# Kernel optimization log

Hardware: AMD Instinct MI355X
Metric: run time of the kernel (lower is better)

Reference implementation:

```python
import jax, jax.numpy as jnp
import numpy as np
from jax import lax

B, S, L, E, H, V = 32, 64, 256, 64, 64, 6000


def setup_inputs() -> dict:
    key = jax.random.key(0)
    ks = jax.random.split(key, 8)
    inp = {
        "ids": jax.random.randint(ks[0], (B, S, L), 0, V, dtype=jnp.int32),
        "embed_table": jax.random.normal(ks[1], (V, E), jnp.float32) * 0.05,
        "Wk_f": jax.random.normal(ks[2], (E, 4 * H), jnp.float32) * 0.05,
        "Wr_f": jax.random.normal(ks[3], (H, 4 * H), jnp.float32) * 0.05,
        "b_f": jnp.zeros((4 * H,), jnp.float32),
        "Wk_b": jax.random.normal(ks[4], (E, 4 * H), jnp.float32) * 0.05,
        "Wr_b": jax.random.normal(ks[5], (H, 4 * H), jnp.float32) * 0.05,
        "b_b": jnp.zeros((4 * H,), jnp.float32),
    }
    return inp


def _lstm(xs, Wk, Wr, b):
    # xs: [L, N, E] -> hidden states [L, N, H]; Keras LSTM gate order i,f,c,o
    N = xs.shape[1]
    Hh = Wr.shape[0]
    pre = jnp.einsum('lne,eg->lng', xs, Wk) + b  # input projection once, outside scan

    def step(carry, zt):
        h, c = carry
        z = zt + h @ Wr
        i, f, g, o = jnp.split(z, 4, axis=-1)
        i = jax.nn.sigmoid(i)
        f = jax.nn.sigmoid(f)
        g = jnp.tanh(g)
        o = jax.nn.sigmoid(o)
        c = f * c + i * g
        h = o * jnp.tanh(c)
        return (h, c), h

    h0 = jnp.zeros((N, Hh), xs.dtype)
    _, hs = lax.scan(step, (h0, h0), pre)
    return hs


def reference(ids, embed_table, Wk_f, Wr_f, b_f, Wk_b, Wr_b, b_b):
    b, s, l = ids.shape
    e = embed_table.shape[1]
    h = Wr_f.shape[0]
    x = embed_table[ids]                      # [B,S,L,E]
    xs = x.reshape(b * s, l, e).transpose(1, 0, 2)  # [L, B*S, E]
    h_fwd = _lstm(xs, Wk_f, Wr_f, b_f)              # [L, N, H]
    h_bwd = _lstm(xs[::-1], Wk_b, Wr_b, b_b)[::-1]  # [L, N, H]
    out = jnp.concatenate([h_fwd, h_bwd], axis=-1)  # [L, N, 2H]
    return out.transpose(1, 0, 2).reshape(b, s, l, 2 * h)
```

## Files before the change

### kernel.cpp

```cpp
#include <hip/hip_runtime.h>

#define LL 256
#define EE 64
#define HH 64
#define GG 256
#define NSEQ 8
#define MROW 16
#define ROWP 72

typedef __bf16 bf16_t;
typedef bf16_t bf16x8 __attribute__((ext_vector_type(8)));
typedef float  f32x4  __attribute__((ext_vector_type(4)));

union BfPack {
    unsigned short u[8];
    bf16x8 v;
};

__device__ __forceinline__ unsigned short f2bf(float f) {
    return __builtin_bit_cast(unsigned short, (__bf16)f);
}

#define LOG2E 1.44269504088896340736f

__device__ __forceinline__ float sigm(float x) {
    float e = __builtin_amdgcn_exp2f(-LOG2E * x);
    return __builtin_amdgcn_rcpf(1.0f + e);
}
__device__ __forceinline__ float tanh_fast(float x) {
    float e = __builtin_amdgcn_exp2f((2.0f * LOG2E) * x);
    return 1.0f - 2.0f * __builtin_amdgcn_rcpf(e + 1.0f);
}

#define LGKM_BARRIER() asm volatile("s_waitcnt lgkmcnt(0)\n\ts_barrier" ::: "memory")

__global__ __launch_bounds__(256, 2)
void bilstm_mfma(const int* __restrict__ ids,
                 const float* __restrict__ embed,
                 const float* __restrict__ Wk_f, const float* __restrict__ Wr_f,
                 const float* __restrict__ b_f,
                 const float* __restrict__ Wk_b, const float* __restrict__ Wr_b,
                 const float* __restrict__ b_b,
                 float* __restrict__ out)
{
    const int dir = blockIdx.x >> 8;
    const int grp = blockIdx.x & 255;
    const int n0  = grp * NSEQ;
    const int tid  = threadIdx.x;
    const int w    = tid >> 6;
    const int lane = tid & 63;
    const int l15  = lane & 15;
    const int quad = lane >> 4;
    const int j    = w * 16 + l15;

    const float* Wk = dir ? Wk_b : Wk_f;
    const float* Wr = dir ? Wr_b : Wr_f;
    const float* bv = dir ? b_b  : b_f;

    __shared__ __align__(16) short s_x[2][MROW][ROWP];
    __shared__ __align__(16) short s_h[2][MROW][ROWP];
    __shared__ int s_ids[NSEQ][LL];

    for (int p = tid; p < NSEQ * LL; p += 256) {
        int m = p >> 8, t = p & 255;
        s_ids[m][t] = ids[(size_t)(n0 + m) * LL + t];
    }
    for (int p = tid; p < 2 * MROW * ROWP; p += 256) {
        (&s_h[0][0][0])[p] = 0;
        (&s_x[0][0][0])[p] = 0;
    }

    __syncthreads();

    bf16x8 bfrag[4][4];
    f32x4  biasC[4];
    #pragma unroll
    for (int tt = 0; tt < 4; ++tt) {
        int g = tt * 64 + j;
        float bb = bv[g];
        biasC[tt] = (f32x4){bb, bb, bb, bb};
        #pragma unroll
        for (int kc = 0; kc < 4; ++kc) {
            BfPack pk;
            #pragma unroll
            for (int e = 0; e < 8; ++e) {
                int kg = kc * 32 + quad * 8 + e;
                float v = (kg < 64) ? Wk[(size_t)kg * GG + g]
                                    : Wr[(size_t)(kg - 64) * GG + g];
                pk.u[e] = f2bf(v);
            }
            bfrag[tt][kc] = pk.v;
        }
    }

    {
        int t0 = dir ? (LL - 1) : 0;
        int m = tid >> 5, ep = tid & 31;
        int id = s_ids[m][t0];
        float2 xv = *(const float2*)&embed[(size_t)id * EE + 2 * ep];
        unsigned pk = (unsigned)f2bf(xv.x) | ((unsigned)f2bf(xv.y) << 16);
        *(unsigned*)&s_x[0][m][2 * ep] = pk;
    }
    __syncthreads();

    float c[4] = {0.f, 0.f, 0.f, 0.f};
    const f32x4 zero4 = (f32x4){0.f, 0.f, 0.f, 0.f};

    const int tstep = dir ? -(2 * HH) : (2 * HH);
    float* optr[4];
    {
        const int t0 = dir ? (LL - 1) : 0;
        #pragma unroll
        for (int r = 0; r < 4; ++r) {
            int m = quad * 4 + r;
            int mm = (m < NSEQ) ? m : 0;
            optr[r] = out + ((size_t)(n0 + mm) * LL + t0) * (2 * HH) + dir * HH + j;
        }
    }

    for (int ts = 0; ts < LL; ++ts) {
        const int rb = ts & 1, wb = (ts + 1) & 1;

        float2 px0;
        const int pm0 = tid >> 5, pe = tid & 31;
        const bool pf = (ts + 1 < LL);
        if (pf) {
            int tn = dir ? (LL - 2 - ts) : (ts + 1);
            px0 = *(const float2*)&embed[(size_t)s_ids[pm0][tn] * EE + 2 * pe];
        }

        bf16x8 ax0 = *(const bf16x8*)&s_x[rb][l15][quad * 8];
        bf16x8 ax1 = *(const bf16x8*)&s_x[rb][l15][32 + quad * 8];
        bf16x8 ah0 = *(const bf16x8*)&s_h[rb][l15][quad * 8];
        bf16x8 ah1 = *(const bf16x8*)&s_h[rb][l15][32 + quad * 8];

        f32x4 acc[4];
        #pragma unroll
        for (int tt = 0; tt < 4; ++tt) {
            f32x4 axc = __builtin_amdgcn_mfma_f32_16x16x32_bf16(ax0, bfrag[tt][0], biasC[tt], 0, 0, 0);
            axc = __builtin_amdgcn_mfma_f32_16x16x32_bf16(ax1, bfrag[tt][1], axc, 0, 0, 0);
            f32x4 ahc = __builtin_amdgcn_mfma_f32_16x16x32_bf16(ah0, bfrag[tt][2], zero4, 0, 0, 0);
            ahc = __builtin_amdgcn_mfma_f32_16x16x32_bf16(ah1, bfrag[tt][3], ahc, 0, 0, 0);
            acc[tt] = axc + ahc;
        }

        #pragma unroll
        for (int r = 0; r < 4; ++r) {
            float ig = sigm(acc[0][r]);
            float fg = sigm(acc[1][r]);
            float gg = tanh_fast(acc[2][r]);
            float og = sigm(acc[3][r]);
            c[r] = fg * c[r] + ig * gg;
            float hh = og * tanh_fast(c[r]);
            if (quad < 2) {
                *optr[r] = hh;
                s_h[wb][quad * 4 + r][j] = (short)f2bf(hh);
            }
            optr[r] += tstep;
        }

        if (pf) {
            unsigned pk0 = (unsigned)f2bf(px0.x) | ((unsigned)f2bf(px0.y) << 16);
            *(unsigned*)&s_x[wb][pm0][2 * pe] = pk0;
        }
        LGKM_BARRIER();
    }
}

extern "C" void kernel_launch(void* const* d_in, const int* in_sizes, int n_in,
                              void* d_out, int out_size, void* d_ws, size_t ws_size,
                              hipStream_t stream) {
    const int*   ids   = (const int*)d_in[0];
    const float* embed = (const float*)d_in[1];
    const float* Wk_f  = (const float*)d_in[2];
    const float* Wr_f  = (const float*)d_in[3];
    const float* b_f   = (const float*)d_in[4];
    const float* Wk_b  = (const float*)d_in[5];
    const float* Wr_b  = (const float*)d_in[6];
    const float* b_b   = (const float*)d_in[7];
    float* out = (float*)d_out;

    dim3 grid(512);
    dim3 block(256);
    bilstm_mfma<<<grid, block, 0, stream>>>(ids, embed,
                                            Wk_f, Wr_f, b_f,
                                            Wk_b, Wr_b, b_b,
                                            out);
}
```

Measured before the change: 476.3 us.

## Precompute vocab-level input projection table and pack 16 sequences per block

Adds a pre-kernel that computes embed_table @ Wk + b for every vocabulary entry and direction into a workspace table laid out to match the MFMA accumulator layout. The recurrent kernel then gathers precomputed gate pre-activations by token id and feeds them as the MFMA accumulator input, which halves the MFMAs per step. Each block now handles 16 sequences instead of 8, so all 16 MFMA rows are used, with 256 blocks at one block per CU. The trade-offs are a larger per-step gather (1 KB fp32 rows per token) and an extra kernel launch. The grid also halves, which reduces parallelism across CUs.

```diff
diff --git a/kernel.cpp b/kernel.cpp
--- a/kernel.cpp
+++ b/kernel.cpp
@@ -4,9 +4,10 @@
 #define EE 64
 #define HH 64
 #define GG 256
-#define NSEQ 8
-#define MROW 16
+#define VV 6000
+#define NSEQ 16
 #define ROWP 72
+#define VBLK 375
 
 typedef __bf16 bf16_t;
 typedef bf16_t bf16x8 __attribute__((ext_vector_type(8)));
@@ -34,17 +35,67 @@
 
 #define LGKM_BARRIER() asm volatile("s_waitcnt lgkmcnt(0)\n\ts_barrier" ::: "memory")
 
-__global__ __launch_bounds__(256, 2)
+__global__ __launch_bounds__(256)
+void embed_pre_kernel(const float* __restrict__ embed,
+                      const float* __restrict__ Wk_f, const float* __restrict__ b_f,
+                      const float* __restrict__ Wk_b, const float* __restrict__ b_b,
+                      float* __restrict__ pre)
+{
+    const int bid = blockIdx.x;
+    const int dir = bid / VBLK;
+    const int v0  = (bid % VBLK) * 16;
+    const float* Wk = dir ? Wk_b : Wk_f;
+    const float* bv = dir ? b_b  : b_f;
+    float* dst = pre + (size_t)dir * VV * GG;
+
+    const int tid = threadIdx.x;
+    const int r   = tid >> 4;
+    const int cg  = tid & 15;
+
+    __shared__ float sW[16][GG];
+    __shared__ float sE[16][17];
+
+    float acc[16];
+    #pragma unroll
+    for (int k = 0; k < 16; ++k) acc[k] = 0.f;
+
+    for (int ec = 0; ec < 4; ++ec) {
+        {
+            int er = tid >> 4;
+            int c0 = (tid & 15) * 16;
+            const float* src = &Wk[(size_t)(ec * 16 + er) * GG + c0];
+            *(float4*)&sW[er][c0 + 0]  = *(const float4*)(src + 0);
+            *(float4*)&sW[er][c0 + 4]  = *(const float4*)(src + 4);
+            *(float4*)&sW[er][c0 + 8]  = *(const float4*)(src + 8);
+            *(float4*)&sW[er][c0 + 12] = *(const float4*)(src + 12);
+            sE[er][tid & 15] = embed[(size_t)(v0 + er) * EE + ec * 16 + (tid & 15)];
+        }
+        __syncthreads();
+        #pragma unroll
+        for (int e = 0; e < 16; ++e) {
+            float xe = sE[r][e];
+            #pragma unroll
+            for (int k = 0; k < 16; ++k)
+                acc[k] += xe * sW[e][k * 16 + cg];
+        }
+        __syncthreads();
+    }
+    #pragma unroll
+    for (int k = 0; k < 16; ++k) {
+        int g = k * 16 + cg;
+        int pos = ((g >> 4) & 3) * 64 + (g & 15) * 4 + (g >> 6);
+        dst[(size_t)(v0 + r) * GG + pos] = acc[k] + bv[g];
+    }
+}
+
+__global__ __launch_bounds__(256, 1)
 void bilstm_mfma(const int* __restrict__ ids,
-                 const float* __restrict__ embed,
-                 const float* __restrict__ Wk_f, const float* __restrict__ Wr_f,
-                 const float* __restrict__ b_f,
-                 const float* __restrict__ Wk_b, const float* __restrict__ Wr_b,
-                 const float* __restrict__ b_b,
+                 const float* __restrict__ Wr_f, const float* __restrict__ Wr_b,
+                 const float* __restrict__ pre,
                  float* __restrict__ out)
 {
-    const int dir = blockIdx.x >> 8;
-    const int grp = blockIdx.x & 255;
+    const int dir = blockIdx.x >> 7;
+    const int grp = blockIdx.x & 127;
     const int n0  = grp * NSEQ;
     const int tid  = threadIdx.x;
     const int w    = tid >> 6;
@@ -53,95 +104,82 @@
     const int quad = lane >> 4;
     const int j    = w * 16 + l15;
 
-    const float* Wk = dir ? Wk_b : Wk_f;
     const float* Wr = dir ? Wr_b : Wr_f;
-    const float* bv = dir ? b_b  : b_f;
-
-    __shared__ __align__(16) short s_x[2][MROW][ROWP];
-    __shared__ __align__(16) short s_h[2][MROW][ROWP];
-    __shared__ int s_ids[NSEQ][LL];
+    const float* preT = pre + (size_t)dir * VV * GG;
+    const int coff = w * 64 + l15 * 4;
+
+    __shared__ __align__(16) short s_h[2][NSEQ][ROWP];
+    __shared__ int s_ids[NSEQ][LL + 1];
 
     for (int p = tid; p < NSEQ * LL; p += 256) {
         int m = p >> 8, t = p & 255;
         s_ids[m][t] = ids[(size_t)(n0 + m) * LL + t];
     }
-    for (int p = tid; p < 2 * MROW * ROWP; p += 256) {
+    for (int p = tid; p < 2 * NSEQ * ROWP; p += 256)
         (&s_h[0][0][0])[p] = 0;
-        (&s_x[0][0][0])[p] = 0;
-    }
 
     __syncthreads();
 
-    bf16x8 bfrag[4][4];
-    f32x4  biasC[4];
+    bf16x8 bfrag[4][2];
     #pragma unroll
     for (int tt = 0; tt < 4; ++tt) {
         int g = tt * 64 + j;
-        float bb = bv[g];
-        biasC[tt] = (f32x4){bb, bb, bb, bb};
-        #pragma unroll
-        for (int kc = 0; kc < 4; ++kc) {
+        #pragma unroll
+        for (int kc = 0; kc < 2; ++kc) {
             BfPack pk;
             #pragma unroll
             for (int e = 0; e < 8; ++e) {
                 int kg = kc * 32 + quad * 8 + e;
-                float v = (kg < 64) ? Wk[(size_t)kg * GG + g]
-                                    : Wr[(size_t)(kg - 64) * GG + g];
-                pk.u[e] = f2bf(v);
+                pk.u[e] = f2bf(Wr[(size_t)kg * GG + g]);
             }
             bfrag[tt][kc] = pk.v;
         }
     }
 
+    f32x4 curP[4];
     {
         int t0 = dir ? (LL - 1) : 0;
-        int m = tid >> 5, ep = tid & 31;
-        int id = s_ids[m][t0];
-        float2 xv = *(const float2*)&embed[(size_t)id * EE + 2 * ep];
-        unsigned pk = (unsigned)f2bf(xv.x) | ((unsigned)f2bf(xv.y) << 16);
-        *(unsigned*)&s_x[0][m][2 * ep] = pk;
-    }
-    __syncthreads();
+        #pragma unroll
+        for (int r = 0; r < 4; ++r) {
+            int id = s_ids[quad * 4 + r][t0];
+            curP[r] = *(const f32x4*)&preT[(size_t)id * GG + coff];
+        }
+    }
 
     float c[4] = {0.f, 0.f, 0.f, 0.f};
-    const f32x4 zero4 = (f32x4){0.f, 0.f, 0.f, 0.f};
 
     const int tstep = dir ? -(2 * HH) : (2 * HH);
     float* optr[4];
     {
         const int t0 = dir ? (LL - 1) : 0;
         #pragma unroll
-        for (int r = 0; r < 4; ++r) {
-            int m = quad * 4 + r;
-            int mm = (m < NSEQ) ? m : 0;
-            optr[r] = out + ((size_t)(n0 + mm) * LL + t0) * (2 * HH) + dir * HH + j;
-        }
+        for (int r = 0; r < 4; ++r)
+            optr[r] = out + ((size_t)(n0 + quad * 4 + r) * LL + t0) * (2 * HH) + dir * HH + j;
     }
 
     for (int ts = 0; ts < LL; ++ts) {
         const int rb = ts & 1, wb = (ts + 1) & 1;
 
-        float2 px0;
-        const int pm0 = tid >> 5, pe = tid & 31;
+        f32x4 nxtP[4];
         const bool pf = (ts + 1 < LL);
         if (pf) {
             int tn = dir ? (LL - 2 - ts) : (ts + 1);
-            px0 = *(const float2*)&embed[(size_t)s_ids[pm0][tn] * EE + 2 * pe];
-        }
-
-        bf16x8 ax0 = *(const bf16x8*)&s_x[rb][l15][quad * 8];
-        bf16x8 ax1 = *(const bf16x8*)&s_x[rb][l15][32 + quad * 8];
+            #pragma unroll
+            for (int r = 0; r < 4; ++r) {
+                int id = s_ids[quad * 4 + r][tn];
+                nxtP[r] = *(const f32x4*)&preT[(size_t)id * GG + coff];
+            }
+        }
+
         bf16x8 ah0 = *(const bf16x8*)&s_h[rb][l15][quad * 8];
         bf16x8 ah1 = *(const bf16x8*)&s_h[rb][l15][32 + quad * 8];
 
         f32x4 acc[4];
         #pragma unroll
         for (int tt = 0; tt < 4; ++tt) {
-            f32x4 axc = __builtin_amdgcn_mfma_f32_16x16x32_bf16(ax0, bfrag[tt][0], biasC[tt], 0, 0, 0);
-            axc = __builtin_amdgcn_mfma_f32_16x16x32_bf16(ax1, bfrag[tt][1], axc, 0, 0, 0);
-            f32x4 ahc = __builtin_amdgcn_mfma_f32_16x16x32_bf16(ah0, bfrag[tt][2], zero4, 0, 0, 0);
-            ahc = __builtin_amdgcn_mfma_f32_16x16x32_bf16(ah1, bfrag[tt][3], ahc, 0, 0, 0);
-            acc[tt] = axc + ahc;
+            f32x4 cIn = (f32x4){curP[0][tt], curP[1][tt], curP[2][tt], curP[3][tt]};
+            f32x4 a = __builtin_amdgcn_mfma_f32_16x16x32_bf16(ah0, bfrag[tt][0], cIn, 0, 0, 0);
+            acc[tt]  = __builtin_amdgcn_mfma_f32_16x16x32_bf16(ah1, bfrag[tt][1], a, 0, 0, 0);
         }
 
         #pragma unroll
@@ -152,17 +190,14 @@
             float og = sigm(acc[3][r]);
             c[r] = fg * c[r] + ig * gg;
             float hh = og * tanh_fast(c[r]);
-            if (quad < 2) {
-                *optr[r] = hh;
-                s_h[wb][quad * 4 + r][j] = (short)f2bf(hh);
-            }
+            *optr[r] = hh;
             optr[r] += tstep;
-        }
-
-        if (pf) {
-            unsigned pk0 = (unsigned)f2bf(px0.x) | ((unsigned)f2bf(px0.y) << 16);
-            *(unsigned*)&s_x[wb][pm0][2 * pe] = pk0;
-        }
+            s_h[wb][quad * 4 + r][j] = (short)f2bf(hh);
+        }
+
+        #pragma unroll
+        for (int r = 0; r < 4; ++r) curP[r] = nxtP[r];
+
         LGKM_BARRIER();
     }
 }
@@ -179,11 +214,10 @@
     const float* Wr_b  = (const float*)d_in[6];
     const float* b_b   = (const float*)d_in[7];
     float* out = (float*)d_out;
-
-    dim3 grid(512);
-    dim3 block(256);
-    bilstm_mfma<<<grid, block, 0, stream>>>(ids, embed,
-                                            Wk_f, Wr_f, b_f,
-                                            Wk_b, Wr_b, b_b,
-                                            out);
-}
+    float* pre = (float*)d_ws;
+
+    embed_pre_kernel<<<dim3(2 * VBLK), dim3(256), 0, stream>>>(
+        embed, Wk_f, b_f, Wk_b, b_b, pre);
+
+    bilstm_mfma<<<dim3(256), dim3(256), 0, stream>>>(ids, Wr_f, Wr_b, pre, out);
+}
```

Measured after the change: 430.9 us. 1.11x faster.
